# Optimization experiments

Hardware: AMD Instinct MI355X
Metric: run time of the kernel (lower is better)

## Reference

```python
import jax, jax.numpy as jnp
import numpy as np

T, S, R, K, O = 10, 10, 2000, 100, 500  # times, subjects, reads/sample, assemblages, otus
EPS = 1e-6


def setup_inputs() -> dict:
    key = jax.random.key(0)
    k1, k2, k3 = jax.random.split(key, 3)
    # nonnegative read counts per (time, subject, particle, otu)
    counts = jax.random.uniform(k1, (T, S, R, O), dtype=jnp.float32) * 10.0
    theta_params = jax.random.normal(k2, (K, O), dtype=jnp.float32)
    beta = jax.random.uniform(k3, (K, T, S), dtype=jnp.float32)
    beta = beta / jnp.sum(beta, axis=0, keepdims=True)  # simplex over assemblages
    return {"counts": counts, "theta_params": theta_params, "beta": beta}


def reference(counts, theta_params, beta):
    # theta: assemblage-wise OTU distributions
    theta = jax.nn.softmax(theta_params, axis=1)              # [K, O]
    logtheta = jnp.log(theta + EPS)                           # [K, O]
    # rlogtheta[t,s,r,k] = sum_o counts[t,s,r,o] * log(theta[k,o] + EPS)
    rlog = jnp.einsum('tsro,ko->tsrk', counts, logtheta)      # [T, S, R, K]
    # stable logsumexp over assemblages, weighted by beta[k, t, s]
    x_star = jnp.max(rlog, axis=-1, keepdims=True)            # [T, S, R, 1]
    b = jnp.transpose(beta, (1, 2, 0))[:, :, None, :]         # [T, S, 1, K]
    summand = x_star[..., 0] + jnp.log(
        jnp.sum(b * jnp.exp(rlog - x_star), axis=-1) + EPS)   # [T, S, R]
    loglik = jnp.sum(summand)
    # use_contamination=False path: pi=None, KL_pi=0; KL_beta external -> 0 here
    elbo_loss = -loglik
    return (elbo_loss, theta, beta)
```

## Files before the change

### kernel.cpp

```cpp
#include <hip/hip_runtime.h>
#include <math.h>

#define TT 10
#define SS 10
#define RR 2000
#define KK 100
#define OO 500
#define PP (TT*SS*RR)
#define NTILES (PP/16)
#define NT 7
#define NWAVES_TOTAL 4096
#define EPSF 1e-6f

typedef float        f32x4  __attribute__((ext_vector_type(4)));
typedef unsigned int u32x4  __attribute__((ext_vector_type(4)));
typedef __bf16       bf16x8 __attribute__((ext_vector_type(8)));

union BFU { bf16x8 v; u32x4 q; };

__device__ __forceinline__ int swz(int row, int byteInRow) {
    return row * 1024 + (byteInRow ^ ((row & 7) << 4));
}

__global__ __launch_bounds__(64) void mcspace_prep(
    const float* __restrict__ theta_params,
    const float* __restrict__ beta,
    float* __restrict__ out)
{
    const int b  = blockIdx.x;
    const int ln = threadIdx.x;
    if (b < KK) {
        const float* tp = theta_params + b * OO;
        float x[8];
        #pragma unroll
        for (int j = 0; j < 8; ++j) {
            int o = ln + 64 * j;
            x[j] = (o < OO) ? tp[o] : -INFINITY;
        }
        float mx = x[0];
        #pragma unroll
        for (int j = 1; j < 8; ++j) mx = fmaxf(mx, x[j]);
        #pragma unroll
        for (int w = 1; w < 64; w <<= 1) mx = fmaxf(mx, __shfl_xor(mx, w));
        float e[8], sm = 0.f;
        #pragma unroll
        for (int j = 0; j < 8; ++j) { e[j] = __expf(x[j] - mx); sm += e[j]; }
        #pragma unroll
        for (int w = 1; w < 64; w <<= 1) sm += __shfl_xor(sm, w);
        const float inv = 1.f / sm;
        float* to = out + 1 + b * OO;
        #pragma unroll
        for (int j = 0; j < 8; ++j) {
            int o = ln + 64 * j;
            if (o < OO) to[o] = e[j] * inv;
        }
    } else {
        int idx = (b - KK) * 64 + ln;
        if (idx < KK * TT * SS) out[1 + KK * OO + idx] = beta[idx];
        if (b == KK && ln == 0) out[0] = 0.f;
    }
}

__global__ __launch_bounds__(1024) void mcspace_main(
    const float* __restrict__ counts,
    const float* __restrict__ theta_params,
    const float* __restrict__ beta,
    float* __restrict__ out)
{
    __shared__ u32x4 ldsB[7168];
    __shared__ float red[16];
    char* ldsBytes = (char*)&ldsB[0];

    const int tid = threadIdx.x;
    const int wv  = tid >> 6;
    const int ln  = tid & 63;
    const int lo  = ln & 15;
    const int g   = ln >> 4;

    for (int it = 0; it < 7; ++it) {
        const int row = wv + 16 * it;
        BFU w8; w8.q = (u32x4){0u, 0u, 0u, 0u};
        if (row < KK) {
            const float* tp = theta_params + row * OO;
            float x[8];
            #pragma unroll
            for (int j = 0; j < 8; ++j) {
                int o = ln * 8 + j;
                x[j] = (o < OO) ? tp[o] : -INFINITY;
            }
            float mx = x[0];
            #pragma unroll
            for (int j = 1; j < 8; ++j) mx = fmaxf(mx, x[j]);
            #pragma unroll
            for (int w = 1; w < 64; w <<= 1) mx = fmaxf(mx, __shfl_xor(mx, w));
            float e[8], sm = 0.f;
            #pragma unroll
            for (int j = 0; j < 8; ++j) { e[j] = __expf(x[j] - mx); sm += e[j]; }
            #pragma unroll
            for (int w = 1; w < 64; w <<= 1) sm += __shfl_xor(sm, w);
            const float inv = 1.f / sm;
            #pragma unroll
            for (int j = 0; j < 8; ++j)
                w8.v[j] = (__bf16)__logf(e[j] * inv + EPSF);
        }
        *(u32x4*)(ldsBytes + swz(row, ln * 16)) = w8.q;
    }
    __syncthreads();

    float wacc = 0.f;
    const int gw = blockIdx.x * 16 + wv;
    const int kb = g * 8;

    for (int tile = gw; tile < NTILES; tile += NWAVES_TOTAL) {
        const int pbase = tile * 16;
        const int ts = pbase / RR;
        const float* rp = counts + (long)(pbase + lo) * OO;

        float bet[NT];
        #pragma unroll
        for (int nt = 0; nt < NT; ++nt) {
            int j = nt * 16 + lo;
            bet[nt] = (j < KK) ? beta[j * (TT * SS) + ts] : 0.f;
        }

        f32x4 acc[NT];
        #pragma unroll
        for (int nt = 0; nt < NT; ++nt) acc[nt] = (f32x4){0.f, 0.f, 0.f, 0.f};

        #pragma unroll 3
        for (int ko = 0; ko < 15; ++ko) {
            f32x4 a0 = *(const f32x4*)(rp + ko * 32 + kb);
            f32x4 a1 = *(const f32x4*)(rp + ko * 32 + kb + 4);
            BFU a;
            #pragma unroll
            for (int j = 0; j < 4; ++j) {
                a.v[j]     = (__bf16)a0[j];
                a.v[4 + j] = (__bf16)a1[j];
            }
            const int bb = ko * 64 + g * 16;
            #pragma unroll
            for (int nt = 0; nt < NT; ++nt) {
                BFU bv;
                bv.q = *(const u32x4*)(ldsBytes + swz(nt * 16 + lo, bb));
                acc[nt] = __builtin_amdgcn_mfma_f32_16x16x32_bf16(a.v, bv.v, acc[nt], 0, 0, 0);
            }
        }
        {
            BFU a;
            #pragma unroll
            for (int j = 0; j < 8; ++j) {
                int k = 480 + kb + j;
                a.v[j] = (__bf16)((k < OO) ? rp[k] : 0.f);
            }
            const int bb = 15 * 64 + g * 16;
            #pragma unroll
            for (int nt = 0; nt < NT; ++nt) {
                BFU bv;
                bv.q = *(const u32x4*)(ldsBytes + swz(nt * 16 + lo, bb));
                acc[nt] = __builtin_amdgcn_mfma_f32_16x16x32_bf16(a.v, bv.v, acc[nt], 0, 0, 0);
            }
        }

        float mrow[4] = {-INFINITY, -INFINITY, -INFINITY, -INFINITY};
        #pragma unroll
        for (int nt = 0; nt < NT; ++nt) {
            const bool valid = (nt * 16 + lo) < KK;
            #pragma unroll
            for (int r = 0; r < 4; ++r) {
                float v = valid ? acc[nt][r] : -INFINITY;
                mrow[r] = fmaxf(mrow[r], v);
            }
        }
        #pragma unroll
        for (int w = 1; w < 16; w <<= 1) {
            #pragma unroll
            for (int r = 0; r < 4; ++r)
                mrow[r] = fmaxf(mrow[r], __shfl_xor(mrow[r], w));
        }
        float srow[4] = {0.f, 0.f, 0.f, 0.f};
        #pragma unroll
        for (int nt = 0; nt < NT; ++nt) {
            const bool valid = (nt * 16 + lo) < KK;
            #pragma unroll
            for (int r = 0; r < 4; ++r) {
                float v = valid ? (acc[nt][r] - mrow[r]) : -INFINITY;
                srow[r] += bet[nt] * __expf(v);
            }
        }
        #pragma unroll
        for (int w = 1; w < 16; w <<= 1) {
            #pragma unroll
            for (int r = 0; r < 4; ++r)
                srow[r] += __shfl_xor(srow[r], w);
        }
        if (lo == 0) {
            #pragma unroll
            for (int r = 0; r < 4; ++r)
                wacc += mrow[r] + __logf(srow[r] + EPSF);
        }
    }

    #pragma unroll
    for (int w = 1; w < 64; w <<= 1) wacc += __shfl_xor(wacc, w);
    if (ln == 0) red[wv] = wacc;
    __syncthreads();
    if (tid == 0) {
        float s = 0.f;
        #pragma unroll
        for (int i = 0; i < 16; ++i) s += red[i];
        atomicAdd(out, -s);
    }
}

extern "C" void kernel_launch(void* const* d_in, const int* in_sizes, int n_in,
                              void* d_out, int out_size, void* d_ws, size_t ws_size,
                              hipStream_t stream)
{
    (void)in_sizes; (void)n_in; (void)d_ws; (void)ws_size; (void)out_size;
    const float* counts       = (const float*)d_in[0];
    const float* theta_params = (const float*)d_in[1];
    const float* beta         = (const float*)d_in[2];
    float* out = (float*)d_out;

    mcspace_prep<<<dim3(KK + (KK * TT * SS + 63) / 64), dim3(64), 0, stream>>>(
        theta_params, beta, out);
    mcspace_main<<<dim3(256), dim3(1024), 0, stream>>>(
        counts, theta_params, beta, out);
}
```

Measured before the change: 139.2 us.

## Process two 16-row tiles per wave to reuse LDS theta fragments, shrink blocks

Measured after the change: 156.1 us. +12.2%, slower.

```diff
diff --git a/kernel.cpp b/kernel.cpp
--- a/kernel.cpp
+++ b/kernel.cpp
@@ -7,9 +7,11 @@
 #define KK 100
 #define OO 500
 #define PP (TT*SS*RR)
-#define NTILES (PP/16)
+#define NUNITS 6250
 #define NT 7
-#define NWAVES_TOTAL 4096
+#define WAVES 12
+#define BLOCKT (WAVES*64)
+#define NWAVES_TOTAL (256*WAVES)
 #define EPSF 1e-6f
 
 typedef float        f32x4  __attribute__((ext_vector_type(4)));
@@ -61,14 +63,14 @@
     }
 }
 
-__global__ __launch_bounds__(1024) void mcspace_main(
+__global__ __launch_bounds__(BLOCKT) void mcspace_main(
     const float* __restrict__ counts,
     const float* __restrict__ theta_params,
     const float* __restrict__ beta,
     float* __restrict__ out)
 {
     __shared__ u32x4 ldsB[7168];
-    __shared__ float red[16];
+    __shared__ float red[WAVES];
     char* ldsBytes = (char*)&ldsB[0];
 
     const int tid = threadIdx.x;
@@ -77,8 +79,9 @@
     const int lo  = ln & 15;
     const int g   = ln >> 4;
 
-    for (int it = 0; it < 7; ++it) {
-        const int row = wv + 16 * it;
+    for (int it = 0; it < 10; ++it) {
+        const int row = wv + WAVES * it;
+        if (row >= 112) break;
         BFU w8; w8.q = (u32x4){0u, 0u, 0u, 0u};
         if (row < KK) {
             const float* tp = theta_params + row * OO;
@@ -108,95 +111,112 @@
     __syncthreads();
 
     float wacc = 0.f;
-    const int gw = blockIdx.x * 16 + wv;
+    const int gw = blockIdx.x * WAVES + wv;
     const int kb = g * 8;
 
-    for (int tile = gw; tile < NTILES; tile += NWAVES_TOTAL) {
-        const int pbase = tile * 16;
+    for (int unit = gw; unit < NUNITS; unit += NWAVES_TOTAL) {
+        const int pbase = unit * 32;
         const int ts = pbase / RR;
-        const float* rp = counts + (long)(pbase + lo) * OO;
-
-        float bet[NT];
-        #pragma unroll
-        for (int nt = 0; nt < NT; ++nt) {
-            int j = nt * 16 + lo;
-            bet[nt] = (j < KK) ? beta[j * (TT * SS) + ts] : 0.f;
-        }
-
-        f32x4 acc[NT];
-        #pragma unroll
-        for (int nt = 0; nt < NT; ++nt) acc[nt] = (f32x4){0.f, 0.f, 0.f, 0.f};
+        const float* rp0 = counts + (long)(pbase + lo) * OO;
+        const float* rp1 = rp0 + 16 * OO;
+
+        f32x4 acc0[NT], acc1[NT];
+        #pragma unroll
+        for (int nt = 0; nt < NT; ++nt) {
+            acc0[nt] = (f32x4){0.f, 0.f, 0.f, 0.f};
+            acc1[nt] = (f32x4){0.f, 0.f, 0.f, 0.f};
+        }
 
         #pragma unroll 3
         for (int ko = 0; ko < 15; ++ko) {
-            f32x4 a0 = *(const f32x4*)(rp + ko * 32 + kb);
-            f32x4 a1 = *(const f32x4*)(rp + ko * 32 + kb + 4);
-            BFU a;
+            f32x4 a0 = *(const f32x4*)(rp0 + ko * 32 + kb);
+            f32x4 a1 = *(const f32x4*)(rp0 + ko * 32 + kb + 4);
+            f32x4 b0 = *(const f32x4*)(rp1 + ko * 32 + kb);
+            f32x4 b1 = *(const f32x4*)(rp1 + ko * 32 + kb + 4);
+            BFU aA, aB;
             #pragma unroll
             for (int j = 0; j < 4; ++j) {
-                a.v[j]     = (__bf16)a0[j];
-                a.v[4 + j] = (__bf16)a1[j];
+                aA.v[j]     = (__bf16)a0[j];
+                aA.v[4 + j] = (__bf16)a1[j];
+                aB.v[j]     = (__bf16)b0[j];
+                aB.v[4 + j] = (__bf16)b1[j];
             }
             const int bb = ko * 64 + g * 16;
             #pragma unroll
             for (int nt = 0; nt < NT; ++nt) {
                 BFU bv;
                 bv.q = *(const u32x4*)(ldsBytes + swz(nt * 16 + lo, bb));
-                acc[nt] = __builtin_amdgcn_mfma_f32_16x16x32_bf16(a.v, bv.v, acc[nt], 0, 0, 0);
+                acc0[nt] = __builtin_amdgcn_mfma_f32_16x16x32_bf16(aA.v, bv.v, acc0[nt], 0, 0, 0);
+                acc1[nt] = __builtin_amdgcn_mfma_f32_16x16x32_bf16(aB.v, bv.v, acc1[nt], 0, 0, 0);
             }
         }
         {
-            BFU a;
+            BFU aA, aB;
             #pragma unroll
             for (int j = 0; j < 8; ++j) {
                 int k = 480 + kb + j;
-                a.v[j] = (__bf16)((k < OO) ? rp[k] : 0.f);
+                aA.v[j] = (__bf16)((k < OO) ? rp0[k] : 0.f);
+                aB.v[j] = (__bf16)((k < OO) ? rp1[k] : 0.f);
             }
             const int bb = 15 * 64 + g * 16;
             #pragma unroll
             for (int nt = 0; nt < NT; ++nt) {
                 BFU bv;
                 bv.q = *(const u32x4*)(ldsBytes + swz(nt * 16 + lo, bb));
-                acc[nt] = __builtin_amdgcn_mfma_f32_16x16x32_bf16(a.v, bv.v, acc[nt], 0, 0, 0);
-            }
-        }
-
-        float mrow[4] = {-INFINITY, -INFINITY, -INFINITY, -INFINITY};
+                acc0[nt] = __builtin_amdgcn_mfma_f32_16x16x32_bf16(aA.v, bv.v, acc0[nt], 0, 0, 0);
+                acc1[nt] = __builtin_amdgcn_mfma_f32_16x16x32_bf16(aB.v, bv.v, acc1[nt], 0, 0, 0);
+            }
+        }
+
+        float bet[NT];
+        #pragma unroll
+        for (int nt = 0; nt < NT; ++nt) {
+            int j = nt * 16 + lo;
+            bet[nt] = (j < KK) ? beta[j * (TT * SS) + ts] : 0.f;
+        }
+
+        float mA[4] = {-INFINITY, -INFINITY, -INFINITY, -INFINITY};
+        float mB[4] = {-INFINITY, -INFINITY, -INFINITY, -INFINITY};
         #pragma unroll
         for (int nt = 0; nt < NT; ++nt) {
             const bool valid = (nt * 16 + lo) < KK;
             #pragma unroll
             for (int r = 0; r < 4; ++r) {
-                float v = valid ? acc[nt][r] : -INFINITY;
-                mrow[r] = fmaxf(mrow[r], v);
+                mA[r] = fmaxf(mA[r], valid ? acc0[nt][r] : -INFINITY);
+                mB[r] = fmaxf(mB[r], valid ? acc1[nt][r] : -INFINITY);
             }
         }
         #pragma unroll
         for (int w = 1; w < 16; w <<= 1) {
             #pragma unroll
+            for (int r = 0; r < 4; ++r) {
+                mA[r] = fmaxf(mA[r], __shfl_xor(mA[r], w));
+                mB[r] = fmaxf(mB[r], __shfl_xor(mB[r], w));
+            }
+        }
+        float sA[4] = {0.f, 0.f, 0.f, 0.f};
+        float sB[4] = {0.f, 0.f, 0.f, 0.f};
+        #pragma unroll
+        for (int nt = 0; nt < NT; ++nt) {
+            const bool valid = (nt * 16 + lo) < KK;
+            #pragma unroll
+            for (int r = 0; r < 4; ++r) {
+                sA[r] += bet[nt] * __expf(valid ? (acc0[nt][r] - mA[r]) : -INFINITY);
+                sB[r] += bet[nt] * __expf(valid ? (acc1[nt][r] - mB[r]) : -INFINITY);
+            }
+        }
+        #pragma unroll
+        for (int w = 1; w < 16; w <<= 1) {
+            #pragma unroll
+            for (int r = 0; r < 4; ++r) {
+                sA[r] += __shfl_xor(sA[r], w);
+                sB[r] += __shfl_xor(sB[r], w);
+            }
+        }
+        if (lo == 0) {
+            #pragma unroll
             for (int r = 0; r < 4; ++r)
-                mrow[r] = fmaxf(mrow[r], __shfl_xor(mrow[r], w));
-        }
-        float srow[4] = {0.f, 0.f, 0.f, 0.f};
-        #pragma unroll
-        for (int nt = 0; nt < NT; ++nt) {
-            const bool valid = (nt * 16 + lo) < KK;
-            #pragma unroll
-            for (int r = 0; r < 4; ++r) {
-                float v = valid ? (acc[nt][r] - mrow[r]) : -INFINITY;
-                srow[r] += bet[nt] * __expf(v);
-            }
-        }
-        #pragma unroll
-        for (int w = 1; w < 16; w <<= 1) {
-            #pragma unroll
-            for (int r = 0; r < 4; ++r)
-                srow[r] += __shfl_xor(srow[r], w);
-        }
-        if (lo == 0) {
-            #pragma unroll
-            for (int r = 0; r < 4; ++r)
-                wacc += mrow[r] + __logf(srow[r] + EPSF);
+                wacc += (mA[r] + __logf(sA[r] + EPSF)) + (mB[r] + __logf(sB[r] + EPSF));
         }
     }
 
@@ -207,7 +227,7 @@
     if (tid == 0) {
         float s = 0.f;
         #pragma unroll
-        for (int i = 0; i < 16; ++i) s += red[i];
+        for (int i = 0; i < WAVES; ++i) s += red[i];
         atomicAdd(out, -s);
     }
 }
@@ -224,6 +244,6 @@
 
     mcspace_prep<<<dim3(KK + (KK * TT * SS + 63) / 64), dim3(64), 0, stream>>>(
         theta_params, beta, out);
-    mcspace_main<<<dim3(256), dim3(1024), 0, stream>>>(
+    mcspace_main<<<dim3(256), dim3(BLOCKT), 0, stream>>>(
         counts, theta_params, beta, out);
 }
```

## Stage counts tiles through LDS with register prefetch and block-cooperative MFMA

Applied to the files above, without the earlier changes.

New measurement: 144.8 us. 1.04x slower.

```diff
diff --git a/kernel.cpp b/kernel.cpp
--- a/kernel.cpp
+++ b/kernel.cpp
@@ -7,16 +7,24 @@
 #define KK 100
 #define OO 500
 #define PP (TT*SS*RR)
-#define NTILES (PP/16)
-#define NT 7
-#define NWAVES_TOTAL 4096
+#define TROWS 32
+#define NTILES (PP/TROWS)
+#define NBLK 256
+#define WAVES 14
+#define BLOCKT (WAVES*64)
+#define CHUNKS 4000
+#define CPT 5
+#define RLP 114
 #define EPSF 1e-6f
 
 typedef float        f32x4  __attribute__((ext_vector_type(4)));
 typedef unsigned int u32x4  __attribute__((ext_vector_type(4)));
+typedef unsigned int u32x2  __attribute__((ext_vector_type(2)));
 typedef __bf16       bf16x8 __attribute__((ext_vector_type(8)));
+typedef __bf16       bf16x4 __attribute__((ext_vector_type(4)));
 
 union BFU { bf16x8 v; u32x4 q; };
+union BF4 { bf16x4 v; u32x2 q; };
 
 __device__ __forceinline__ int swz(int row, int byteInRow) {
     return row * 1024 + (byteInRow ^ ((row & 7) << 4));
@@ -61,24 +69,41 @@
     }
 }
 
-__global__ __launch_bounds__(1024) void mcspace_main(
+__global__ __launch_bounds__(BLOCKT) void mcspace_main(
     const float* __restrict__ counts,
     const float* __restrict__ theta_params,
     const float* __restrict__ beta,
     float* __restrict__ out)
 {
-    __shared__ u32x4 ldsB[7168];
-    __shared__ float red[16];
-    char* ldsBytes = (char*)&ldsB[0];
+    __shared__ u32x4 ldsB[112 * 64];
+    __shared__ u32x4 ldsA[32 * 64];
+    __shared__ float rlog[32 * RLP];
+    __shared__ float betaT[2 * 112];
+    __shared__ float red[WAVES];
+    char* bB = (char*)ldsB;
+    char* bA = (char*)ldsA;
 
     const int tid = threadIdx.x;
     const int wv  = tid >> 6;
     const int ln  = tid & 63;
     const int lo  = ln & 15;
     const int g   = ln >> 4;
-
-    for (int it = 0; it < 7; ++it) {
-        const int row = wv + 16 * it;
+    const int b   = blockIdx.x;
+
+    const int ntile_mine = (NTILES - b + NBLK - 1) / NBLK;
+
+    f32x4 cur[CPT];
+    {
+        long tf = (long)b * (TROWS * OO);
+        #pragma unroll
+        for (int j = 0; j < CPT; ++j) {
+            int c = tid + j * BLOCKT;
+            if (c < CHUNKS) cur[j] = *(const f32x4*)(counts + tf + (long)c * 4);
+        }
+    }
+
+    for (int it = 0; it < 8; ++it) {
+        const int row = wv + WAVES * it;
         BFU w8; w8.q = (u32x4){0u, 0u, 0u, 0u};
         if (row < KK) {
             const float* tp = theta_params + row * OO;
@@ -103,100 +128,96 @@
             for (int j = 0; j < 8; ++j)
                 w8.v[j] = (__bf16)__logf(e[j] * inv + EPSF);
         }
-        *(u32x4*)(ldsBytes + swz(row, ln * 16)) = w8.q;
-    }
-    __syncthreads();
+        *(u32x4*)(bB + swz(row, ln * 16)) = w8.q;
+    }
+
+    if (tid < 32) {
+        const int row = tid;
+        u32x2 z = (u32x2){0u, 0u};
+        *(u32x2*)(bA + swz(row, 1000)) = z;
+        *(u32x2*)(bA + swz(row, 1008)) = z;
+        *(u32x2*)(bA + swz(row, 1016)) = z;
+    }
+
+    const int m  = wv / 7;
+    const int nt = wv % 7;
+    const int xr = (lo & 7) << 4;
+    const int baseAoff = (m * 16 + lo) * 1024;
+    const int baseBoff = (nt * 16 + lo) * 1024;
+    const int g16 = g * 16;
 
     float wacc = 0.f;
-    const int gw = blockIdx.x * 16 + wv;
-    const int kb = g * 8;
-
-    for (int tile = gw; tile < NTILES; tile += NWAVES_TOTAL) {
-        const int pbase = tile * 16;
-        const int ts = pbase / RR;
-        const float* rp = counts + (long)(pbase + lo) * OO;
-
-        float bet[NT];
-        #pragma unroll
-        for (int nt = 0; nt < NT; ++nt) {
-            int j = nt * 16 + lo;
-            bet[nt] = (j < KK) ? beta[j * (TT * SS) + ts] : 0.f;
-        }
-
-        f32x4 acc[NT];
-        #pragma unroll
-        for (int nt = 0; nt < NT; ++nt) acc[nt] = (f32x4){0.f, 0.f, 0.f, 0.f};
-
-        #pragma unroll 3
-        for (int ko = 0; ko < 15; ++ko) {
-            f32x4 a0 = *(const f32x4*)(rp + ko * 32 + kb);
-            f32x4 a1 = *(const f32x4*)(rp + ko * 32 + kb + 4);
-            BFU a;
-            #pragma unroll
-            for (int j = 0; j < 4; ++j) {
-                a.v[j]     = (__bf16)a0[j];
-                a.v[4 + j] = (__bf16)a1[j];
+
+    for (int it = 0; it < ntile_mine; ++it) {
+        const int tile   = b + it * NBLK;
+        const int pbase  = tile * TROWS;
+        const int ts0    = pbase / (RR);
+        const int rb     = (ts0 + 1) * RR - pbase;
+        const int ts1    = ts0 + ((rb < TROWS) ? 1 : 0);
+
+        __syncthreads();
+
+        #pragma unroll
+        for (int j = 0; j < CPT; ++j) {
+            int c = tid + j * BLOCKT;
+            if (c < CHUNKS) {
+                int row = c / 125;
+                int kc  = c % 125;
+                BF4 w;
+                #pragma unroll
+                for (int q = 0; q < 4; ++q) w.v[q] = (__bf16)cur[j][q];
+                *(u32x2*)(bA + swz(row, kc * 8)) = w.q;
             }
-            const int bb = ko * 64 + g * 16;
-            #pragma unroll
-            for (int nt = 0; nt < NT; ++nt) {
-                BFU bv;
-                bv.q = *(const u32x4*)(ldsBytes + swz(nt * 16 + lo, bb));
-                acc[nt] = __builtin_amdgcn_mfma_f32_16x16x32_bf16(a.v, bv.v, acc[nt], 0, 0, 0);
+        }
+
+        if (it + 1 < ntile_mine) {
+            long tf = (long)(tile + NBLK) * (TROWS * OO);
+            #pragma unroll
+            for (int j = 0; j < CPT; ++j) {
+                int c = tid + j * BLOCKT;
+                if (c < CHUNKS) cur[j] = *(const f32x4*)(counts + tf + (long)c * 4);
             }
         }
-        {
-            BFU a;
-            #pragma unroll
-            for (int j = 0; j < 8; ++j) {
-                int k = 480 + kb + j;
-                a.v[j] = (__bf16)((k < OO) ? rp[k] : 0.f);
-            }
-            const int bb = 15 * 64 + g * 16;
-            #pragma unroll
-            for (int nt = 0; nt < NT; ++nt) {
-                BFU bv;
-                bv.q = *(const u32x4*)(ldsBytes + swz(nt * 16 + lo, bb));
-                acc[nt] = __builtin_amdgcn_mfma_f32_16x16x32_bf16(a.v, bv.v, acc[nt], 0, 0, 0);
-            }
-        }
-
-        float mrow[4] = {-INFINITY, -INFINITY, -INFINITY, -INFINITY};
-        #pragma unroll
-        for (int nt = 0; nt < NT; ++nt) {
-            const bool valid = (nt * 16 + lo) < KK;
-            #pragma unroll
-            for (int r = 0; r < 4; ++r) {
-                float v = valid ? acc[nt][r] : -INFINITY;
-                mrow[r] = fmaxf(mrow[r], v);
-            }
-        }
-        #pragma unroll
-        for (int w = 1; w < 16; w <<= 1) {
-            #pragma unroll
-            for (int r = 0; r < 4; ++r)
-                mrow[r] = fmaxf(mrow[r], __shfl_xor(mrow[r], w));
-        }
-        float srow[4] = {0.f, 0.f, 0.f, 0.f};
-        #pragma unroll
-        for (int nt = 0; nt < NT; ++nt) {
-            const bool valid = (nt * 16 + lo) < KK;
-            #pragma unroll
-            for (int r = 0; r < 4; ++r) {
-                float v = valid ? (acc[nt][r] - mrow[r]) : -INFINITY;
-                srow[r] += bet[nt] * __expf(v);
-            }
-        }
-        #pragma unroll
-        for (int w = 1; w < 16; w <<= 1) {
-            #pragma unroll
-            for (int r = 0; r < 4; ++r)
-                srow[r] += __shfl_xor(srow[r], w);
-        }
-        if (lo == 0) {
-            #pragma unroll
-            for (int r = 0; r < 4; ++r)
-                wacc += mrow[r] + __logf(srow[r] + EPSF);
+
+        __syncthreads();
+
+        f32x4 acc = (f32x4){0.f, 0.f, 0.f, 0.f};
+        #pragma unroll
+        for (int ko = 0; ko < 16; ++ko) {
+            const int t = (ko * 64 + g16) ^ xr;
+            BFU av, bv;
+            av.q = *(const u32x4*)(bA + baseAoff + t);
+            bv.q = *(const u32x4*)(bB + baseBoff + t);
+            acc = __builtin_amdgcn_mfma_f32_16x16x32_bf16(av.v, bv.v, acc, 0, 0, 0);
+        }
+
+        #pragma unroll
+        for (int r = 0; r < 4; ++r)
+            rlog[(m * 16 + 4 * g + r) * RLP + nt * 16 + lo] = acc[r];
+
+        if (tid < 112) {
+            betaT[tid] = (tid < KK) ? beta[tid * (TT * SS) + ts0] : 0.f;
+        } else if (tid < 224) {
+            int j = tid - 112;
+            betaT[112 + j] = (j < KK) ? beta[j * (TT * SS) + ts1] : 0.f;
+        }
+
+        __syncthreads();
+
+        for (int row = wv; row < TROWS; row += WAVES) {
+            const int sel = (row >= rb) ? 112 : 0;
+            const float v1 = rlog[row * RLP + ln];
+            const float b1 = betaT[sel + ln];
+            const bool  ok2 = (ln < 36);
+            const float v2 = ok2 ? rlog[row * RLP + 64 + ln] : -INFINITY;
+            const float b2 = ok2 ? betaT[sel + 64 + ln] : 0.f;
+            float mx = fmaxf(v1, v2);
+            #pragma unroll
+            for (int w = 1; w < 64; w <<= 1) mx = fmaxf(mx, __shfl_xor(mx, w));
+            float s = b1 * __expf(v1 - mx) + b2 * __expf(v2 - mx);
+            #pragma unroll
+            for (int w = 1; w < 64; w <<= 1) s += __shfl_xor(s, w);
+            if (ln == 0) wacc += mx + __logf(s + EPSF);
         }
     }
 
@@ -207,7 +228,7 @@
     if (tid == 0) {
         float s = 0.f;
         #pragma unroll
-        for (int i = 0; i < 16; ++i) s += red[i];
+        for (int i = 0; i < WAVES; ++i) s += red[i];
         atomicAdd(out, -s);
     }
 }
@@ -224,6 +245,6 @@
 
     mcspace_prep<<<dim3(KK + (KK * TT * SS + 63) / 64), dim3(64), 0, stream>>>(
         theta_params, beta, out);
-    mcspace_main<<<dim3(256), dim3(1024), 0, stream>>>(
+    mcspace_main<<<dim3(NBLK), dim3(BLOCKT), 0, stream>>>(
         counts, theta_params, beta, out);
 }
```

## Precompute fragment-ordered log-theta in workspace and stage coalesced counts via LDS

Applied to the files above, without the earlier changes.

Result: slower. 535.1 us (+284.4%).

```diff
diff --git a/kernel.cpp b/kernel.cpp
--- a/kernel.cpp
+++ b/kernel.cpp
@@ -7,114 +7,146 @@
 #define KK 100
 #define OO 500
 #define PP (TT*SS*RR)
-#define NTILES (PP/16)
+#define NT16 12500
 #define NT 7
-#define NWAVES_TOTAL 4096
+#define WPB 3
+#define BLOCKT (WPB*64)
+#define NBLK 1536
+#define TOTW (NBLK*WPB)
 #define EPSF 1e-6f
 
 typedef float        f32x4  __attribute__((ext_vector_type(4)));
 typedef unsigned int u32x4  __attribute__((ext_vector_type(4)));
+typedef unsigned int u32x2  __attribute__((ext_vector_type(2)));
 typedef __bf16       bf16x8 __attribute__((ext_vector_type(8)));
+typedef __bf16       bf16x4 __attribute__((ext_vector_type(4)));
 
 union BFU { bf16x8 v; u32x4 q; };
-
-__device__ __forceinline__ int swz(int row, int byteInRow) {
-    return row * 1024 + (byteInRow ^ ((row & 7) << 4));
-}
+union BF4 { bf16x4 v; u32x2 q; };
 
 __global__ __launch_bounds__(64) void mcspace_prep(
     const float* __restrict__ theta_params,
     const float* __restrict__ beta,
+    float* __restrict__ out,
+    u32x4* __restrict__ Bf)
+{
+    __shared__ float row[512];
+    const int b  = blockIdx.x;
+    const int ln = threadIdx.x;
+    if (b < 112) {
+        const int nt = b >> 4, lo = b & 15;
+        const int ko = ln >> 2, g = ln & 3;
+        if (b < KK) {
+            const float* tp = theta_params + b * OO;
+            float x[8];
+            #pragma unroll
+            for (int j = 0; j < 8; ++j) {
+                int o = ln + 64 * j;
+                x[j] = (o < OO) ? tp[o] : -INFINITY;
+            }
+            float mx = x[0];
+            #pragma unroll
+            for (int j = 1; j < 8; ++j) mx = fmaxf(mx, x[j]);
+            #pragma unroll
+            for (int w = 1; w < 64; w <<= 1) mx = fmaxf(mx, __shfl_xor(mx, w));
+            float e[8], sm = 0.f;
+            #pragma unroll
+            for (int j = 0; j < 8; ++j) { e[j] = __expf(x[j] - mx); sm += e[j]; }
+            #pragma unroll
+            for (int w = 1; w < 64; w <<= 1) sm += __shfl_xor(sm, w);
+            const float inv = 1.f / sm;
+            #pragma unroll
+            for (int j = 0; j < 8; ++j) {
+                int o = ln + 64 * j;
+                float th = e[j] * inv;
+                if (o < OO) out[1 + b * OO + o] = th;
+                row[o] = th;
+            }
+            __syncthreads();
+            BFU w8;
+            #pragma unroll
+            for (int i = 0; i < 8; ++i)
+                w8.v[i] = (__bf16)__logf(row[ko * 32 + g * 8 + i] + EPSF);
+            Bf[(ko * 7 + nt) * 64 + g * 16 + lo] = w8.q;
+        } else {
+            Bf[(ko * 7 + nt) * 64 + g * 16 + lo] = (u32x4){0u, 0u, 0u, 0u};
+        }
+    } else {
+        int idx = (b - 112) * 64 + ln;
+        if (idx < KK * TT * SS) out[1 + KK * OO + idx] = beta[idx];
+        if (b == 112 && ln == 0) out[0] = 0.f;
+    }
+}
+
+__global__ __launch_bounds__(BLOCKT, 5) void mcspace_main(
+    const float* __restrict__ counts,
+    const float* __restrict__ beta,
+    const u32x4* __restrict__ Bf,
     float* __restrict__ out)
 {
-    const int b  = blockIdx.x;
-    const int ln = threadIdx.x;
-    if (b < KK) {
-        const float* tp = theta_params + b * OO;
-        float x[8];
-        #pragma unroll
-        for (int j = 0; j < 8; ++j) {
-            int o = ln + 64 * j;
-            x[j] = (o < OO) ? tp[o] : -INFINITY;
-        }
-        float mx = x[0];
-        #pragma unroll
-        for (int j = 1; j < 8; ++j) mx = fmaxf(mx, x[j]);
-        #pragma unroll
-        for (int w = 1; w < 64; w <<= 1) mx = fmaxf(mx, __shfl_xor(mx, w));
-        float e[8], sm = 0.f;
-        #pragma unroll
-        for (int j = 0; j < 8; ++j) { e[j] = __expf(x[j] - mx); sm += e[j]; }
-        #pragma unroll
-        for (int w = 1; w < 64; w <<= 1) sm += __shfl_xor(sm, w);
-        const float inv = 1.f / sm;
-        float* to = out + 1 + b * OO;
-        #pragma unroll
-        for (int j = 0; j < 8; ++j) {
-            int o = ln + 64 * j;
-            if (o < OO) to[o] = e[j] * inv;
-        }
-    } else {
-        int idx = (b - KK) * 64 + ln;
-        if (idx < KK * TT * SS) out[1 + KK * OO + idx] = beta[idx];
-        if (b == KK && ln == 0) out[0] = 0.f;
-    }
-}
-
-__global__ __launch_bounds__(1024) void mcspace_main(
-    const float* __restrict__ counts,
-    const float* __restrict__ theta_params,
-    const float* __restrict__ beta,
-    float* __restrict__ out)
-{
-    __shared__ u32x4 ldsB[7168];
-    __shared__ float red[16];
-    char* ldsBytes = (char*)&ldsB[0];
+    __shared__ char Abuf[WPB][8192];
+    __shared__ float red[WPB];
 
     const int tid = threadIdx.x;
     const int wv  = tid >> 6;
     const int ln  = tid & 63;
     const int lo  = ln & 15;
     const int g   = ln >> 4;
-
-    for (int it = 0; it < 7; ++it) {
-        const int row = wv + 16 * it;
-        BFU w8; w8.q = (u32x4){0u, 0u, 0u, 0u};
-        if (row < KK) {
-            const float* tp = theta_params + row * OO;
-            float x[8];
-            #pragma unroll
-            for (int j = 0; j < 8; ++j) {
-                int o = ln * 8 + j;
-                x[j] = (o < OO) ? tp[o] : -INFINITY;
-            }
-            float mx = x[0];
-            #pragma unroll
-            for (int j = 1; j < 8; ++j) mx = fmaxf(mx, x[j]);
-            #pragma unroll
-            for (int w = 1; w < 64; w <<= 1) mx = fmaxf(mx, __shfl_xor(mx, w));
-            float e[8], sm = 0.f;
-            #pragma unroll
-            for (int j = 0; j < 8; ++j) { e[j] = __expf(x[j] - mx); sm += e[j]; }
-            #pragma unroll
-            for (int w = 1; w < 64; w <<= 1) sm += __shfl_xor(sm, w);
-            const float inv = 1.f / sm;
-            #pragma unroll
-            for (int j = 0; j < 8; ++j)
-                w8.v[j] = (__bf16)__logf(e[j] * inv + EPSF);
-        }
-        *(u32x4*)(ldsBytes + swz(row, ln * 16)) = w8.q;
-    }
-    __syncthreads();
+    char* wb = Abuf[wv];
+
+    const int xr    = (lo & 7) << 4;
+    const int rdoff = lo * 512;
 
     float wacc = 0.f;
-    const int gw = blockIdx.x * 16 + wv;
-    const int kb = g * 8;
-
-    for (int tile = gw; tile < NTILES; tile += NWAVES_TOTAL) {
-        const int pbase = tile * 16;
-        const int ts = pbase / RR;
-        const float* rp = counts + (long)(pbase + lo) * OO;
+    const int gw = blockIdx.x * WPB + wv;
+
+    for (int tile = gw; tile < NT16; tile += TOTW) {
+        const int ts = tile / 125;
+        const float* base = counts + (long)tile * (16 * OO);
+
+        f32x4 acc[NT];
+        #pragma unroll
+        for (int nt = 0; nt < NT; ++nt) acc[nt] = (f32x4){0.f, 0.f, 0.f, 0.f};
+
+        for (int h = 0; h < 2; ++h) {
+            const int c0  = h * 256;
+            const int lim = h ? 60 : 63;
+
+            #pragma unroll
+            for (int rb = 0; rb < 2; ++rb) {
+                f32x4 v[8];
+                #pragma unroll
+                for (int r = 0; r < 8; ++r) {
+                    int row = rb * 8 + r;
+                    if (ln <= lim)
+                        v[r] = *(const f32x4*)(base + row * OO + c0 + ln * 4);
+                }
+                #pragma unroll
+                for (int r = 0; r < 8; ++r) {
+                    int row = rb * 8 + r;
+                    BF4 w;
+                    if (ln <= lim) {
+                        #pragma unroll
+                        for (int q = 0; q < 4; ++q) w.v[q] = (__bf16)v[r][q];
+                    } else {
+                        w.q = (u32x2){0u, 0u};
+                    }
+                    *(u32x2*)(wb + row * 512 + ((ln * 8) ^ ((row & 7) << 4))) = w.q;
+                }
+            }
+
+            #pragma unroll
+            for (int ko = 0; ko < 8; ++ko) {
+                BFU av;
+                av.q = *(const u32x4*)(wb + rdoff + ((ko * 64 + g * 16) ^ xr));
+                const u32x4* bp = Bf + ((h * 8 + ko) * 7) * 64 + ln;
+                #pragma unroll
+                for (int nt = 0; nt < NT; ++nt) {
+                    BFU bv; bv.q = bp[nt * 64];
+                    acc[nt] = __builtin_amdgcn_mfma_f32_16x16x32_bf16(av.v, bv.v, acc[nt], 0, 0, 0);
+                }
+            }
+        }
 
         float bet[NT];
         #pragma unroll
@@ -122,54 +154,13 @@
             int j = nt * 16 + lo;
             bet[nt] = (j < KK) ? beta[j * (TT * SS) + ts] : 0.f;
         }
-
-        f32x4 acc[NT];
-        #pragma unroll
-        for (int nt = 0; nt < NT; ++nt) acc[nt] = (f32x4){0.f, 0.f, 0.f, 0.f};
-
-        #pragma unroll 3
-        for (int ko = 0; ko < 15; ++ko) {
-            f32x4 a0 = *(const f32x4*)(rp + ko * 32 + kb);
-            f32x4 a1 = *(const f32x4*)(rp + ko * 32 + kb + 4);
-            BFU a;
-            #pragma unroll
-            for (int j = 0; j < 4; ++j) {
-                a.v[j]     = (__bf16)a0[j];
-                a.v[4 + j] = (__bf16)a1[j];
-            }
-            const int bb = ko * 64 + g * 16;
-            #pragma unroll
-            for (int nt = 0; nt < NT; ++nt) {
-                BFU bv;
-                bv.q = *(const u32x4*)(ldsBytes + swz(nt * 16 + lo, bb));
-                acc[nt] = __builtin_amdgcn_mfma_f32_16x16x32_bf16(a.v, bv.v, acc[nt], 0, 0, 0);
-            }
-        }
-        {
-            BFU a;
-            #pragma unroll
-            for (int j = 0; j < 8; ++j) {
-                int k = 480 + kb + j;
-                a.v[j] = (__bf16)((k < OO) ? rp[k] : 0.f);
-            }
-            const int bb = 15 * 64 + g * 16;
-            #pragma unroll
-            for (int nt = 0; nt < NT; ++nt) {
-                BFU bv;
-                bv.q = *(const u32x4*)(ldsBytes + swz(nt * 16 + lo, bb));
-                acc[nt] = __builtin_amdgcn_mfma_f32_16x16x32_bf16(a.v, bv.v, acc[nt], 0, 0, 0);
-            }
-        }
-
         float mrow[4] = {-INFINITY, -INFINITY, -INFINITY, -INFINITY};
         #pragma unroll
         for (int nt = 0; nt < NT; ++nt) {
             const bool valid = (nt * 16 + lo) < KK;
             #pragma unroll
-            for (int r = 0; r < 4; ++r) {
-                float v = valid ? acc[nt][r] : -INFINITY;
-                mrow[r] = fmaxf(mrow[r], v);
-            }
+            for (int r = 0; r < 4; ++r)
+                mrow[r] = fmaxf(mrow[r], valid ? acc[nt][r] : -INFINITY);
         }
         #pragma unroll
         for (int w = 1; w < 16; w <<= 1) {
@@ -182,10 +173,8 @@
         for (int nt = 0; nt < NT; ++nt) {
             const bool valid = (nt * 16 + lo) < KK;
             #pragma unroll
-            for (int r = 0; r < 4; ++r) {
-                float v = valid ? (acc[nt][r] - mrow[r]) : -INFINITY;
-                srow[r] += bet[nt] * __expf(v);
-            }
+            for (int r = 0; r < 4; ++r)
+                srow[r] += bet[nt] * __expf(valid ? (acc[nt][r] - mrow[r]) : -INFINITY);
         }
         #pragma unroll
         for (int w = 1; w < 16; w <<= 1) {
@@ -207,7 +196,7 @@
     if (tid == 0) {
         float s = 0.f;
         #pragma unroll
-        for (int i = 0; i < 16; ++i) s += red[i];
+        for (int i = 0; i < WPB; ++i) s += red[i];
         atomicAdd(out, -s);
     }
 }
@@ -216,14 +205,15 @@
                               void* d_out, int out_size, void* d_ws, size_t ws_size,
                               hipStream_t stream)
 {
-    (void)in_sizes; (void)n_in; (void)d_ws; (void)ws_size; (void)out_size;
+    (void)in_sizes; (void)n_in; (void)ws_size; (void)out_size;
     const float* counts       = (const float*)d_in[0];
     const float* theta_params = (const float*)d_in[1];
     const float* beta         = (const float*)d_in[2];
     float* out = (float*)d_out;
-
-    mcspace_prep<<<dim3(KK + (KK * TT * SS + 63) / 64), dim3(64), 0, stream>>>(
-        theta_params, beta, out);
-    mcspace_main<<<dim3(256), dim3(1024), 0, stream>>>(
-        counts, theta_params, beta, out);
+    u32x4* Bf  = (u32x4*)d_ws;
+
+    mcspace_prep<<<dim3(112 + (KK * TT * SS + 63) / 64), dim3(64), 0, stream>>>(
+        theta_params, beta, out, Bf);
+    mcspace_main<<<dim3(NBLK), dim3(BLOCKT), 0, stream>>>(
+        counts, beta, Bf, out);
 }
```
